# Performance work log

Hardware: AMD Instinct MI355X
Metric: run time of the kernel (lower is better)

Reference implementation:

```python
import jax, jax.numpy as jnp
import numpy as np

B = 65536      # batch (groups of time steps)
T = 5          # time_step
OBS = 128      # unit-data feature dim
ACT = 32       # action feature dim
H = 64         # n_hidden
EPS = 1e-12    # tf.contrib layer_norm epsilon
FORGET_BIAS = 1.0


def _ln_last(x, g, b):
    # layer norm over last axis (2D inputs in the TF graph)
    m = jnp.mean(x, axis=-1, keepdims=True)
    v = jnp.mean(jnp.square(x - m), axis=-1, keepdims=True)
    return (x - m) * jax.lax.rsqrt(v + EPS) * g + b


def _ln_all_but_batch(x, g, b):
    # tf.contrib.layers.layer_norm on 3D input: normalize over axes (1,2), params on last axis
    m = jnp.mean(x, axis=(1, 2), keepdims=True)
    v = jnp.mean(jnp.square(x - m), axis=(1, 2), keepdims=True)
    return (x - m) * jax.lax.rsqrt(v + EPS) * g + b


def _rev_seq(x, au):
    # tf.reverse_sequence along time axis 1 with per-batch lengths au
    t = jnp.arange(T)[None, :]
    idx = jnp.where(t < au[:, None], au[:, None] - 1 - t, t)  # [B, T]
    return jnp.take_along_axis(x, idx[:, :, None], axis=1)


def _lstm(x_btc, au, kernel, bias):
    # BasicLSTMCell (gates i, j, f, o) with sequence_length semantics:
    # past the length, outputs are zero and state is copied through.
    x_tbc = jnp.transpose(x_btc, (1, 0, 2))  # [T, B, C]
    Bn = x_tbc.shape[1]
    c0 = jnp.zeros((Bn, H), x_btc.dtype)
    h0 = jnp.zeros((Bn, H), x_btc.dtype)

    def step(carry, inp):
        c, h = carry
        x_t, t = inp
        valid = (t < au)[:, None]
        gates = jnp.concatenate([x_t, h], axis=-1) @ kernel + bias
        i, j, f, o = jnp.split(gates, 4, axis=-1)
        new_c = jax.nn.sigmoid(f + FORGET_BIAS) * c + jax.nn.sigmoid(i) * jnp.tanh(j)
        new_h = jax.nn.sigmoid(o) * jnp.tanh(new_c)
        c = jnp.where(valid, new_c, c)
        h_carry = jnp.where(valid, new_h, h)
        out = jnp.where(valid, new_h, 0.0)
        return (c, h_carry), out

    (_, _), ys = jax.lax.scan(step, (c0, h0), (x_tbc, jnp.arange(T)))
    return jnp.transpose(ys, (1, 0, 2))  # [B, T, H]


def setup_inputs() -> dict:
    key = jax.random.key(0)
    ks = jax.random.split(key, 12)
    s = 0.05
    return {
        "ud": jax.random.normal(ks[0], (B * T, OBS), jnp.float32),
        "action": jax.random.normal(ks[1], (B * T, ACT), jnp.float32),
        "mask": jax.random.uniform(ks[2], (B, T), jnp.float32),
        "ln0_g": jnp.ones((OBS,), jnp.float32), "ln0_b": jnp.zeros((OBS,), jnp.float32),
        "W1": jax.random.normal(ks[3], (OBS, H), jnp.float32) * s, "b1": jnp.zeros((H,), jnp.float32),
        "ln1_g": jnp.ones((H,), jnp.float32), "ln1_b": jnp.zeros((H,), jnp.float32),
        "W2": jax.random.normal(ks[4], (H + ACT, H), jnp.float32) * s, "b2": jnp.zeros((H,), jnp.float32),
        "ln2_g": jnp.ones((H,), jnp.float32), "ln2_b": jnp.zeros((H,), jnp.float32),
        "fw_k": jax.random.normal(ks[5], (2 * H, 4 * H), jnp.float32) * s,
        "fw_b": jnp.zeros((4 * H,), jnp.float32),
        "bw_k": jax.random.normal(ks[6], (2 * H, 4 * H), jnp.float32) * s,
        "bw_b": jnp.zeros((4 * H,), jnp.float32),
        "ln3_g": jnp.ones((2 * H,), jnp.float32), "ln3_b": jnp.zeros((2 * H,), jnp.float32),
        "conv_w": jax.random.uniform(ks[7], (2 * H,), jnp.float32, -0.003, 0.003),
        "conv_b": jnp.zeros((), jnp.float32),
        "au": jax.random.randint(ks[8], (B,), 1, T + 1, jnp.int32),
    }


def reference(ud, action, mask, ln0_g, ln0_b, W1, b1, ln1_g, ln1_b, W2, b2,
              ln2_g, ln2_b, fw_k, fw_b, bw_k, bw_b, ln3_g, ln3_b,
              conv_w, conv_b, au):
    x = _ln_last(ud, ln0_g, ln0_b)
    x = x @ W1 + b1
    x = jax.nn.relu(_ln_last(x, ln1_g, ln1_b))
    x = jnp.concatenate([x, action], axis=-1)
    x = x @ W2 + b2
    x = jax.nn.relu(_ln_last(x, ln2_g, ln2_b))
    x = x.reshape(B, T, H)
    fw = _lstm(x, au, fw_k, fw_b)
    bw = _rev_seq(_lstm(_rev_seq(x, au), au, bw_k, bw_b), au)
    x = jnp.concatenate([fw, bw], axis=2)                     # [B, T, 2H]
    x = jax.nn.relu(_ln_all_but_batch(x, ln3_g, ln3_b))
    # conv1d with kernel_size=stride=2H on [B, T*2H, 1] == per-step dot product
    q = jnp.einsum('btc,c->bt', x, conv_w) + conv_b           # [B, T]
    Q_mask = q * mask
    Q = jnp.sum(Q_mask, axis=1, keepdims=True)                # [B, 1]
    return Q


if __name__ == "__main__":
    out = reference(**setup_inputs())
    print(out.shape)
```

## Files before the change

kernel.cpp:

```cpp
#include <hip/hip_runtime.h>
#include <hip/hip_bf16.h>

#define NB    65536
#define NT    5
#define NOBS  128
#define NACT  32
#define NH    64

typedef __attribute__((ext_vector_type(8))) short bf16x8;
typedef __attribute__((ext_vector_type(4))) float f32x4;

__device__ __forceinline__ float sigf(float x) { return 1.0f / (1.0f + __expf(-x)); }
__device__ __forceinline__ float tanh_fast(float x) { return 1.0f - 2.0f / (__expf(2.0f * x) + 1.0f); }

__device__ __forceinline__ unsigned short f2b(float x) {
  __hip_bfloat16 h = __float2bfloat16(x);
  return *(unsigned short*)&h;
}
__device__ __forceinline__ float b2f(unsigned short u) {
  __hip_bfloat16 h = *(__hip_bfloat16*)&u;
  return __bfloat162float(h);
}
__device__ __forceinline__ void split_bf16(float x, unsigned short& h, unsigned short& l) {
  h = f2b(x);
  l = f2b(x - b2f(h));
}

__global__ __launch_bounds__(256) void k0_prep(
    const float* __restrict__ fk, const float* __restrict__ bk,
    const float* __restrict__ W1, const float* __restrict__ W2,
    const float* __restrict__ ln0g, const float* __restrict__ ln0b,
    const float* __restrict__ b1,
    unsigned int* __restrict__ fkT, unsigned int* __restrict__ bkT,
    unsigned short* __restrict__ w1h, unsigned short* __restrict__ w1l,
    unsigned short* __restrict__ w2h, unsigned short* __restrict__ w2l,
    float* __restrict__ u1, float* __restrict__ vb1) {
  const int bx = blockIdx.x;
  if (bx < 64) {
    const int g  = threadIdx.x;
    const int k0 = bx * 2;
    unsigned int flo = f2b(fk[(k0 + 0) * 256 + g]);
    unsigned int fhi = f2b(fk[(k0 + 1) * 256 + g]);
    unsigned int blo = f2b(bk[(k0 + 0) * 256 + g]);
    unsigned int bhi = f2b(bk[(k0 + 1) * 256 + g]);
    fkT[g * 64 + bx] = flo | (fhi << 16);
    bkT[g * 64 + bx] = blo | (bhi << 16);
    return;
  }
  const int id = (bx - 64) * 256 + threadIdx.x;
  if (id < 1024) {
    const int f = id >> 6, l = id & 63;
    const int kb = f >> 2, nt = f & 3;
    const int q = l >> 4, l16 = l & 15;
    const int n = nt * 16 + l16;
    bf16x8 vh, vl;
#pragma unroll
    for (int j = 0; j < 8; ++j) {
      const int k = kb * 32 + q * 8 + j;
      float wg = ln0g[k] * W1[k * 64 + n];
      unsigned short h, lo;
      split_bf16(wg, h, lo);
      vh[j] = (short)h; vl[j] = (short)lo;
    }
    *(bf16x8*)&w1h[(f * 64 + l) * 8] = vh;
    *(bf16x8*)&w1l[(f * 64 + l) * 8] = vl;
  } else if (id < 1792) {
    const int f = (id - 1024) >> 6, l = id & 63;
    const int kb = f >> 2, nt = f & 3;
    const int q = l >> 4, l16 = l & 15;
    const int n = nt * 16 + l16;
    bf16x8 vh, vl;
#pragma unroll
    for (int j = 0; j < 8; ++j) {
      const int k = kb * 32 + q * 8 + j;
      float wv = W2[k * 64 + n];
      unsigned short h, lo;
      split_bf16(wv, h, lo);
      vh[j] = (short)h; vl[j] = (short)lo;
    }
    *(bf16x8*)&w2h[(f * 64 + l) * 8] = vh;
    *(bf16x8*)&w2l[(f * 64 + l) * 8] = vl;
  } else if (id < 1856) {
    const int n = id - 1792;
    float u = 0.0f, vb = 0.0f;
    for (int k = 0; k < 128; ++k) {
      float wv = W1[k * 64 + n];
      u  += ln0g[k] * wv;
      vb += ln0b[k] * wv;
    }
    u1[n]  = u;
    vb1[n] = vb + b1[n];
  }
}

__global__ __launch_bounds__(256, 2) void k1_mlp(
    const float* __restrict__ ud, const float* __restrict__ action,
    const unsigned short* __restrict__ w1h, const unsigned short* __restrict__ w1l,
    const unsigned short* __restrict__ w2h, const unsigned short* __restrict__ w2l,
    const float* __restrict__ u1, const float* __restrict__ vb1,
    const float* __restrict__ gb2, const float* __restrict__ ln1g,
    const float* __restrict__ ln1b, const float* __restrict__ ln2g,
    const float* __restrict__ ln2b,
    unsigned short* __restrict__ hin) {
  const int wave = threadIdx.x >> 6;
  const int lane = threadIdx.x & 63;
  const int quad = lane >> 4;
  const int l16  = lane & 15;
  const int base = (blockIdx.x * 4 + wave) * 16;

  __shared__ __align__(16) unsigned short lds[4][4][2048];
  unsigned short* xh  = &lds[wave][0][0];
  unsigned short* xl  = &lds[wave][1][0];
  unsigned short* x2h = &lds[wave][2][0];
  unsigned short* x2l = &lds[wave][3][0];

  float u1v[4], vbv[4], g1v[4], c1v[4], b2v[4], g2v[4], c2v[4];
#pragma unroll
  for (int nt = 0; nt < 4; ++nt) {
    const int col = nt * 16 + l16;
    u1v[nt] = u1[col];  vbv[nt] = vb1[col];
    g1v[nt] = ln1g[col]; c1v[nt] = ln1b[col];
    b2v[nt] = gb2[col];
    g2v[nt] = ln2g[col]; c2v[nt] = ln2b[col];
  }

  {
    const int arow = lane >> 2, ag = lane & 3;
    const float* ap = &action[(size_t)(base + arow) * NACT + ag * 8];
    float4 a0 = *(const float4*)ap;
    float4 a1 = *(const float4*)(ap + 4);
    float av[8] = {a0.x, a0.y, a0.z, a0.w, a1.x, a1.y, a1.z, a1.w};
    bf16x8 vh, vl;
#pragma unroll
    for (int j = 0; j < 8; ++j) {
      unsigned short h, lo;
      split_bf16(av[j], h, lo);
      vh[j] = (short)h; vl[j] = (short)lo;
    }
    const int idx = arow * 128 + (((8 + ag) ^ (arow & 15)) << 3);
    *(bf16x8*)&x2h[idx] = vh;
    *(bf16x8*)&x2l[idx] = vl;
  }

#pragma unroll
  for (int r = 0; r < 16; ++r) {
    float2 xx = *(const float2*)&ud[(size_t)(base + r) * NOBS + 2 * lane];
    unsigned short h0, l0, h1, l1;
    split_bf16(xx.x, h0, l0);
    split_bf16(xx.y, h1, l1);
    const int di = r * 64 + (((lane >> 2) ^ (r & 15)) << 2) + (lane & 3);
    ((unsigned int*)xh)[di] = (unsigned int)h0 | ((unsigned int)h1 << 16);
    ((unsigned int*)xl)[di] = (unsigned int)l0 | ((unsigned int)l1 << 16);
  }

  bf16x8 W1hf[16], W1lf[16];
#pragma unroll
  for (int f = 0; f < 16; ++f) {
    W1hf[f] = *(const bf16x8*)&w1h[(f * 64 + lane) * 8];
    W1lf[f] = *(const bf16x8*)&w1l[(f * 64 + lane) * 8];
  }

  bf16x8 ones;
#pragma unroll
  for (int j = 0; j < 8; ++j) ones[j] = (short)0x3F80;

  f32x4 acc[4], s_acc, q_acc;
#pragma unroll
  for (int nt = 0; nt < 4; ++nt) acc[nt] = 0.0f;
  s_acc = 0.0f; q_acc = 0.0f;

#pragma unroll
  for (int kb = 0; kb < 4; ++kb) {
    const int ai = l16 * 128 + (((kb * 4 + quad) ^ l16) << 3);
    bf16x8 Ah = *(const bf16x8*)&xh[ai];
    bf16x8 Al = *(const bf16x8*)&xl[ai];
    bf16x8 Asq;
#pragma unroll
    for (int j = 0; j < 8; ++j) {
      unsigned int uu = ((unsigned int)(unsigned short)Ah[j]) << 16;
      float v = __uint_as_float(uu);
      v *= v;
      Asq[j] = (short)(unsigned short)(__float_as_uint(v) >> 16);
    }
    s_acc = __builtin_amdgcn_mfma_f32_16x16x32_bf16(Ah, ones, s_acc, 0, 0, 0);
    s_acc = __builtin_amdgcn_mfma_f32_16x16x32_bf16(Al, ones, s_acc, 0, 0, 0);
    q_acc = __builtin_amdgcn_mfma_f32_16x16x32_bf16(Asq, ones, q_acc, 0, 0, 0);
#pragma unroll
    for (int nt = 0; nt < 4; ++nt) {
      const int f = kb * 4 + nt;
      acc[nt] = __builtin_amdgcn_mfma_f32_16x16x32_bf16(Ah, W1hf[f], acc[nt], 0, 0, 0);
      acc[nt] = __builtin_amdgcn_mfma_f32_16x16x32_bf16(Ah, W1lf[f], acc[nt], 0, 0, 0);
      acc[nt] = __builtin_amdgcn_mfma_f32_16x16x32_bf16(Al, W1hf[f], acc[nt], 0, 0, 0);
    }
  }

  float inv0[4], ivm[4];
#pragma unroll
  for (int r = 0; r < 4; ++r) {
    float m   = s_acc[r] * (1.0f / 128.0f);
    float var = q_acc[r] * (1.0f / 128.0f) - m * m;
    float inv = rsqrtf(var + 1e-12f);
    inv0[r] = inv;
    ivm[r]  = inv * m;
  }
  float y[4][4];
#pragma unroll
  for (int nt = 0; nt < 4; ++nt)
#pragma unroll
    for (int r = 0; r < 4; ++r)
      y[nt][r] = fmaf(inv0[r], acc[nt][r], fmaf(-ivm[r], u1v[nt], vbv[nt]));

  float m1[4], i1[4];
#pragma unroll
  for (int r = 0; r < 4; ++r) {
    float s1 = y[0][r] + y[1][r] + y[2][r] + y[3][r];
    float q1 = y[0][r] * y[0][r] + y[1][r] * y[1][r] +
               y[2][r] * y[2][r] + y[3][r] * y[3][r];
#pragma unroll
    for (int off = 1; off <= 8; off <<= 1) {
      s1 += __shfl_xor(s1, off, 64);
      q1 += __shfl_xor(q1, off, 64);
    }
    float mm = s1 * (1.0f / 64.0f);
    m1[r] = mm;
    i1[r] = rsqrtf(q1 * (1.0f / 64.0f) - mm * mm + 1e-12f);
  }

#pragma unroll
  for (int nt = 0; nt < 4; ++nt)
#pragma unroll
    for (int r = 0; r < 4; ++r) {
      float x1 = fmaxf(0.0f, fmaf((y[nt][r] - m1[r]) * i1[r], g1v[nt], c1v[nt]));
      unsigned short h, lo;
      split_bf16(x1, h, lo);
      const int row = quad * 4 + r;
      const int idx = row * 128 + (((nt * 2 + (l16 >> 3)) ^ (row & 15)) << 3) + (l16 & 7);
      x2h[idx] = h;
      x2l[idx] = lo;
    }

  f32x4 acc2[4];
#pragma unroll
  for (int nt = 0; nt < 4; ++nt) acc2[nt] = 0.0f;

#pragma unroll
  for (int kb = 0; kb < 3; ++kb) {
    bf16x8 w2hf[4], w2lf[4];
#pragma unroll
    for (int nt = 0; nt < 4; ++nt) {
      const int f = kb * 4 + nt;
      w2hf[nt] = *(const bf16x8*)&w2h[(f * 64 + lane) * 8];
      w2lf[nt] = *(const bf16x8*)&w2l[(f * 64 + lane) * 8];
    }
    const int ai = l16 * 128 + (((kb * 4 + quad) ^ l16) << 3);
    bf16x8 Ah = *(const bf16x8*)&x2h[ai];
    bf16x8 Al = *(const bf16x8*)&x2l[ai];
#pragma unroll
    for (int nt = 0; nt < 4; ++nt) {
      acc2[nt] = __builtin_amdgcn_mfma_f32_16x16x32_bf16(Ah, w2hf[nt], acc2[nt], 0, 0, 0);
      acc2[nt] = __builtin_amdgcn_mfma_f32_16x16x32_bf16(Ah, w2lf[nt], acc2[nt], 0, 0, 0);
      acc2[nt] = __builtin_amdgcn_mfma_f32_16x16x32_bf16(Al, w2hf[nt], acc2[nt], 0, 0, 0);
    }
  }

  float y2[4][4];
#pragma unroll
  for (int nt = 0; nt < 4; ++nt)
#pragma unroll
    for (int r = 0; r < 4; ++r)
      y2[nt][r] = acc2[nt][r] + b2v[nt];

  float m2[4], i2[4];
#pragma unroll
  for (int r = 0; r < 4; ++r) {
    float s2 = y2[0][r] + y2[1][r] + y2[2][r] + y2[3][r];
    float q2 = y2[0][r] * y2[0][r] + y2[1][r] * y2[1][r] +
               y2[2][r] * y2[2][r] + y2[3][r] * y2[3][r];
#pragma unroll
    for (int off = 1; off <= 8; off <<= 1) {
      s2 += __shfl_xor(s2, off, 64);
      q2 += __shfl_xor(q2, off, 64);
    }
    float mm = s2 * (1.0f / 64.0f);
    m2[r] = mm;
    i2[r] = rsqrtf(q2 * (1.0f / 64.0f) - mm * mm + 1e-12f);
  }

#pragma unroll
  for (int nt = 0; nt < 4; ++nt)
#pragma unroll
    for (int r = 0; r < 4; ++r) {
      float o = fmaxf(0.0f, fmaf((y2[nt][r] - m2[r]) * i2[r], g2v[nt], c2v[nt]));
      const int row = quad * 4 + r;
      hin[(size_t)(base + row) * NH + nt * 16 + l16] = f2b(o);
    }
}

__global__ __launch_bounds__(256, 2) void k23_lstm_final(
    const unsigned short* __restrict__ hin,
    const unsigned short* __restrict__ fkT, const float* __restrict__ fwb,
    const unsigned short* __restrict__ bkT, const float* __restrict__ bwb,
    const int* __restrict__ au,
    const float* __restrict__ ln3g, const float* __restrict__ ln3b,
    const float* __restrict__ conv_w, const float* __restrict__ conv_b,
    const float* __restrict__ mask, float* __restrict__ out) {
  const int tid  = threadIdx.x;
  const int w    = tid >> 6;
  const int lane = tid & 63;
  const int quad = lane >> 4;
  const int l16  = lane & 15;
  const int batch0 = blockIdx.x * 32;

  __shared__ __align__(16) unsigned short obuf[10 * 32 * 64];
  __shared__ __align__(16) unsigned short hA[32 * 64];

  const int u = w * 16 + l16;

  const int aum0 = au[batch0 + l16];
  const int aum1 = au[batch0 + 16 + l16];
  int aur[8];
#pragma unroll
  for (int mt = 0; mt < 2; ++mt)
#pragma unroll
    for (int r = 0; r < 4; ++r)
      aur[mt * 4 + r] = au[batch0 + mt * 16 + quad * 4 + r];

  for (int dir = 0; dir < 2; ++dir) {
    const unsigned short* kT   = dir ? bkT : fkT;
    const float*          bias = dir ? bwb : fwb;

    bf16x8 Bf[4][4];
#pragma unroll
    for (int g = 0; g < 4; ++g) {
      const int n = g * 64 + u;
#pragma unroll
      for (int kb = 0; kb < 4; ++kb)
        Bf[g][kb] = *(const bf16x8*)&kT[n * 128 + kb * 32 + quad * 8];
    }
    const float bg0 = bias[u], bg1 = bias[64 + u];
    const float bg2 = bias[128 + u], bg3 = bias[192 + u];

    __syncthreads();
    *(float4*)&hA[tid * 8] = make_float4(0.f, 0.f, 0.f, 0.f);
    float c_s[8], h_s[8];
#pragma unroll
    for (int i = 0; i < 8; ++i) { c_s[i] = 0.0f; h_s[i] = 0.0f; }
    __syncthreads();

    bf16x8 Ax0[2], Ax1[2];
#pragma unroll
    for (int mt = 0; mt < 2; ++mt) {
      const int m = mt * 16 + l16;
      const int a = mt ? aum1 : aum0;
      const int st = dir ? (a - 1) : 0;
      const size_t rb = ((size_t)(batch0 + m) * NT + st) * NH;
      Ax0[mt] = *(const bf16x8*)&hin[rb + quad * 8];
      Ax1[mt] = *(const bf16x8*)&hin[rb + 32 + quad * 8];
    }

    for (int t = 0; t < NT; ++t) {
      f32x4 acc[2][4];
#pragma unroll
      for (int mt = 0; mt < 2; ++mt)
#pragma unroll
        for (int g = 0; g < 4; ++g) acc[mt][g] = 0.0f;

#pragma unroll
      for (int mt = 0; mt < 2; ++mt) {
        const int m = mt * 16 + l16;
        bf16x8 Ah0 = *(const bf16x8*)&hA[m * 64 + ((quad ^ (m & 7)) << 3)];
        bf16x8 Ah1 = *(const bf16x8*)&hA[m * 64 + (((4 + quad) ^ (m & 7)) << 3)];
#pragma unroll
        for (int g = 0; g < 4; ++g) {
          acc[mt][g] = __builtin_amdgcn_mfma_f32_16x16x32_bf16(Ax0[mt], Bf[g][0], acc[mt][g], 0, 0, 0);
          acc[mt][g] = __builtin_amdgcn_mfma_f32_16x16x32_bf16(Ax1[mt], Bf[g][1], acc[mt][g], 0, 0, 0);
          acc[mt][g] = __builtin_amdgcn_mfma_f32_16x16x32_bf16(Ah0, Bf[g][2], acc[mt][g], 0, 0, 0);
          acc[mt][g] = __builtin_amdgcn_mfma_f32_16x16x32_bf16(Ah1, Bf[g][3], acc[mt][g], 0, 0, 0);
        }
      }

      if (t < NT - 1) {
        const int t2 = t + 1;
#pragma unroll
        for (int mt = 0; mt < 2; ++mt) {
          const int m = mt * 16 + l16;
          const int a = mt ? aum1 : aum0;
          const int st = dir ? ((t2 < a) ? (a - 1 - t2) : t2) : t2;
          const size_t rb = ((size_t)(batch0 + m) * NT + st) * NH;
          Ax0[mt] = *(const bf16x8*)&hin[rb + quad * 8];
          Ax1[mt] = *(const bf16x8*)&hin[rb + 32 + quad * 8];
        }
      }

      __syncthreads();

#pragma unroll
      for (int mt = 0; mt < 2; ++mt) {
#pragma unroll
        for (int r = 0; r < 4; ++r) {
          const int idx = mt * 4 + r;
          const int bl = mt * 16 + quad * 4 + r;
          float gi = acc[mt][0][r] + bg0;
          float gj = acc[mt][1][r] + bg1;
          float gf = acc[mt][2][r] + bg2;
          float go = acc[mt][3][r] + bg3;
          float nc = sigf(gf + 1.0f) * c_s[idx] + sigf(gi) * tanh_fast(gj);
          float nh = sigf(go) * tanh_fast(nc);
          bool valid = t < aur[idx];
          c_s[idx] = valid ? nc : c_s[idx];
          h_s[idx] = valid ? nh : h_s[idx];
          float outv = valid ? nh : 0.0f;
          int pos = dir ? ((t < aur[idx]) ? (aur[idx] - 1 - t) : t) : t;
          obuf[(dir * 5 + pos) * 2048 + bl * 64 + u] = f2b(outv);
          hA[bl * 64 + (((u >> 3) ^ (bl & 7)) << 3) + (u & 7)] = f2b(h_s[idx]);
        }
      }
      __syncthreads();
    }
  }

  const float gl  = ln3g[lane],      gh  = ln3g[64 + lane];
  const float bl3 = ln3b[lane],      bh3 = ln3b[64 + lane];
  const float cwl = conv_w[lane],    cwh = conv_w[64 + lane];
  const float cb  = conv_b[0];

  for (int bb = w * 8; bb < w * 8 + 8; ++bb) {
    const int b = batch0 + bb;
    float v0[NT], v1[NT];
#pragma unroll
    for (int p = 0; p < NT; ++p) {
      v0[p] = b2f(obuf[p * 2048 + bb * 64 + lane]);
      v1[p] = b2f(obuf[(5 + p) * 2048 + bb * 64 + lane]);
    }
    float s = 0.0f, q = 0.0f;
#pragma unroll
    for (int p = 0; p < NT; ++p) {
      s += v0[p] + v1[p];
      q += v0[p] * v0[p] + v1[p] * v1[p];
    }
#pragma unroll
    for (int off = 32; off; off >>= 1) {
      s += __shfl_xor(s, off, 64);
      q += __shfl_xor(q, off, 64);
    }
    float m = s * (1.0f / 640.0f);
    float var = q * (1.0f / 640.0f) - m * m;
    float inv = rsqrtf(var + 1e-12f);

    float mk[NT], masksum = 0.0f;
#pragma unroll
    for (int p = 0; p < NT; ++p) {
      mk[p] = mask[b * NT + p];
      masksum += mk[p];
    }
    float local = 0.0f;
#pragma unroll
    for (int p = 0; p < NT; ++p) {
      float xf = fmaxf(0.0f, (v0[p] - m) * inv * gl + bl3);
      float xb = fmaxf(0.0f, (v1[p] - m) * inv * gh + bh3);
      local += mk[p] * (xf * cwl + xb * cwh);
    }
#pragma unroll
    for (int off = 32; off; off >>= 1) local += __shfl_xor(local, off, 64);
    if (lane == 0) out[b] = local + cb * masksum;
  }
}

extern "C" void kernel_launch(void* const* d_in, const int* in_sizes, int n_in,
                              void* d_out, int out_size, void* d_ws, size_t ws_size,
                              hipStream_t stream) {
  const float* ud     = (const float*)d_in[0];
  const float* action = (const float*)d_in[1];
  const float* mask   = (const float*)d_in[2];
  const float* ln0g   = (const float*)d_in[3];
  const float* ln0b   = (const float*)d_in[4];
  const float* W1     = (const float*)d_in[5];
  const float* b1     = (const float*)d_in[6];
  const float* ln1g   = (const float*)d_in[7];
  const float* ln1b   = (const float*)d_in[8];
  const float* W2     = (const float*)d_in[9];
  const float* b2     = (const float*)d_in[10];
  const float* ln2g   = (const float*)d_in[11];
  const float* ln2b   = (const float*)d_in[12];
  const float* fwk    = (const float*)d_in[13];
  const float* fwb    = (const float*)d_in[14];
  const float* bwk    = (const float*)d_in[15];
  const float* bwb    = (const float*)d_in[16];
  const float* ln3g   = (const float*)d_in[17];
  const float* ln3b   = (const float*)d_in[18];
  const float* conv_w = (const float*)d_in[19];
  const float* conv_b = (const float*)d_in[20];
  const int*   au     = (const int*)d_in[21];

  const size_t n_hin = (size_t)NB * NT * NH;
  unsigned short* wsu   = (unsigned short*)d_ws;
  unsigned short* hin   = wsu;
  unsigned short* fkT   = hin + n_hin;
  unsigned short* bkT   = fkT + 32768;
  unsigned short* w1h   = bkT + 32768;
  unsigned short* w1l   = w1h + 8192;
  unsigned short* w2h   = w1l + 8192;
  unsigned short* w2l   = w2h + 6144;
  float*          u1    = (float*)(w2l + 6144);
  float*          vb1   = u1 + 64;

  float* outf = (float*)d_out;

  k0_prep<<<72, 256, 0, stream>>>(fwk, bwk, W1, W2, ln0g, ln0b, b1,
                                  (unsigned int*)fkT, (unsigned int*)bkT,
                                  w1h, w1l, w2h, w2l, u1, vb1);
  k1_mlp<<<(NB * NT) / 64, 256, 0, stream>>>(ud, action, w1h, w1l, w2h, w2l,
                                             u1, vb1, b2, ln1g, ln1b, ln2g, ln2b,
                                             hin);
  k23_lstm_final<<<NB / 32, 256, 0, stream>>>(hin, fkT, fwb, bkT, bwb, au,
                                              ln3g, ln3b, conv_w, conv_b,
                                              mask, outf);
}
```

Before: 515.9 us.

## Double-buffer LSTM hidden state, fold biases into MFMA init, use fast rcp and raise occupancy

Double-buffers the shared hidden-state tile so each timestep needs one barrier instead of two, and drops the barrier before zeroing the state. The gate biases, including the forget bias, now seed the MFMA accumulators, and sigmoid/tanh use the hardware reciprocal. The output and hidden values are packed to bf16 with a single instruction. Launch bounds go from 2 to 3 blocks per SM, which may force register spills given the large weight fragments held in registers. The final layer-norm/conv epilogue is unrolled to handle two batch rows per iteration so their shuffle reductions interleave.

Result: slower. 562.2 us (+9.0%).

```diff
diff --git a/kernel.cpp b/kernel.cpp
--- a/kernel.cpp
+++ b/kernel.cpp
@@ -10,8 +10,9 @@
 typedef __attribute__((ext_vector_type(8))) short bf16x8;
 typedef __attribute__((ext_vector_type(4))) float f32x4;
 
-__device__ __forceinline__ float sigf(float x) { return 1.0f / (1.0f + __expf(-x)); }
-__device__ __forceinline__ float tanh_fast(float x) { return 1.0f - 2.0f / (__expf(2.0f * x) + 1.0f); }
+__device__ __forceinline__ float rcp_fast(float x) { return __builtin_amdgcn_rcpf(x); }
+__device__ __forceinline__ float sigf(float x) { return rcp_fast(1.0f + __expf(-x)); }
+__device__ __forceinline__ float tanh_fast(float x) { return 1.0f - 2.0f * rcp_fast(__expf(2.0f * x) + 1.0f); }
 
 __device__ __forceinline__ unsigned short f2b(float x) {
   __hip_bfloat16 h = __float2bfloat16(x);
@@ -296,7 +297,7 @@
     }
 }
 
-__global__ __launch_bounds__(256, 2) void k23_lstm_final(
+__global__ __launch_bounds__(256, 3) void k23_lstm_final(
     const unsigned short* __restrict__ hin,
     const unsigned short* __restrict__ fkT, const float* __restrict__ fwb,
     const unsigned short* __restrict__ bkT, const float* __restrict__ bwb,
@@ -312,7 +313,7 @@
   const int batch0 = blockIdx.x * 32;
 
   __shared__ __align__(16) unsigned short obuf[10 * 32 * 64];
-  __shared__ __align__(16) unsigned short hA[32 * 64];
+  __shared__ __align__(16) unsigned short hA[2][32 * 64];
 
   const int u = w * 16 + l16;
 
@@ -338,10 +339,9 @@
         Bf[g][kb] = *(const bf16x8*)&kT[n * 128 + kb * 32 + quad * 8];
     }
     const float bg0 = bias[u], bg1 = bias[64 + u];
-    const float bg2 = bias[128 + u], bg3 = bias[192 + u];
-
-    __syncthreads();
-    *(float4*)&hA[tid * 8] = make_float4(0.f, 0.f, 0.f, 0.f);
+    const float bg2 = bias[128 + u] + 1.0f, bg3 = bias[192 + u];
+
+    *(float4*)&hA[0][tid * 8] = make_float4(0.f, 0.f, 0.f, 0.f);
     float c_s[8], h_s[8];
 #pragma unroll
     for (int i = 0; i < 8; ++i) { c_s[i] = 0.0f; h_s[i] = 0.0f; }
@@ -358,18 +358,20 @@
       Ax1[mt] = *(const bf16x8*)&hin[rb + 32 + quad * 8];
     }
 
+    int cur = 0;
     for (int t = 0; t < NT; ++t) {
+      const int nxt = cur ^ 1;
       f32x4 acc[2][4];
 #pragma unroll
-      for (int mt = 0; mt < 2; ++mt)
-#pragma unroll
-        for (int g = 0; g < 4; ++g) acc[mt][g] = 0.0f;
+      for (int mt = 0; mt < 2; ++mt) {
+        acc[mt][0] = bg0; acc[mt][1] = bg1; acc[mt][2] = bg2; acc[mt][3] = bg3;
+      }
 
 #pragma unroll
       for (int mt = 0; mt < 2; ++mt) {
         const int m = mt * 16 + l16;
-        bf16x8 Ah0 = *(const bf16x8*)&hA[m * 64 + ((quad ^ (m & 7)) << 3)];
-        bf16x8 Ah1 = *(const bf16x8*)&hA[m * 64 + (((4 + quad) ^ (m & 7)) << 3)];
+        bf16x8 Ah0 = *(const bf16x8*)&hA[cur][m * 64 + ((quad ^ (m & 7)) << 3)];
+        bf16x8 Ah1 = *(const bf16x8*)&hA[cur][m * 64 + (((4 + quad) ^ (m & 7)) << 3)];
 #pragma unroll
         for (int g = 0; g < 4; ++g) {
           acc[mt][g] = __builtin_amdgcn_mfma_f32_16x16x32_bf16(Ax0[mt], Bf[g][0], acc[mt][g], 0, 0, 0);
@@ -392,30 +394,33 @@
         }
       }
 
-      __syncthreads();
-
 #pragma unroll
       for (int mt = 0; mt < 2; ++mt) {
 #pragma unroll
         for (int r = 0; r < 4; ++r) {
           const int idx = mt * 4 + r;
           const int bl = mt * 16 + quad * 4 + r;
-          float gi = acc[mt][0][r] + bg0;
-          float gj = acc[mt][1][r] + bg1;
-          float gf = acc[mt][2][r] + bg2;
-          float go = acc[mt][3][r] + bg3;
-          float nc = sigf(gf + 1.0f) * c_s[idx] + sigf(gi) * tanh_fast(gj);
+          const int a  = aur[idx];
+          float gi = acc[mt][0][r];
+          float gj = acc[mt][1][r];
+          float gf = acc[mt][2][r];
+          float go = acc[mt][3][r];
+          float nc = sigf(gf) * c_s[idx] + sigf(gi) * tanh_fast(gj);
           float nh = sigf(go) * tanh_fast(nc);
-          bool valid = t < aur[idx];
+          bool valid = t < a;
           c_s[idx] = valid ? nc : c_s[idx];
           h_s[idx] = valid ? nh : h_s[idx];
           float outv = valid ? nh : 0.0f;
-          int pos = dir ? ((t < aur[idx]) ? (aur[idx] - 1 - t) : t) : t;
-          obuf[(dir * 5 + pos) * 2048 + bl * 64 + u] = f2b(outv);
-          hA[bl * 64 + (((u >> 3) ^ (bl & 7)) << 3) + (u & 7)] = f2b(h_s[idx]);
+          int pos = dir ? (valid ? (a - 1 - t) : t) : t;
+          unsigned int pk;
+          asm("v_cvt_pk_bf16_f32 %0, %1, %2" : "=v"(pk) : "v"(outv), "v"(h_s[idx]));
+          obuf[(dir * 5 + pos) * 2048 + bl * 64 + u] = (unsigned short)pk;
+          hA[nxt][bl * 64 + (((u >> 3) ^ (bl & 7)) << 3) + (u & 7)] =
+              (unsigned short)(pk >> 16);
         }
       }
       __syncthreads();
+      cur = nxt;
     }
   }
 
@@ -424,45 +429,59 @@
   const float cwl = conv_w[lane],    cwh = conv_w[64 + lane];
   const float cb  = conv_b[0];
 
-  for (int bb = w * 8; bb < w * 8 + 8; ++bb) {
-    const int b = batch0 + bb;
-    float v0[NT], v1[NT];
-#pragma unroll
-    for (int p = 0; p < NT; ++p) {
-      v0[p] = b2f(obuf[p * 2048 + bb * 64 + lane]);
-      v1[p] = b2f(obuf[(5 + p) * 2048 + bb * 64 + lane]);
-    }
-    float s = 0.0f, q = 0.0f;
-#pragma unroll
-    for (int p = 0; p < NT; ++p) {
-      s += v0[p] + v1[p];
-      q += v0[p] * v0[p] + v1[p] * v1[p];
+  for (int bb = w * 8; bb < w * 8 + 8; bb += 2) {
+    float v0[2][NT], v1[2][NT];
+#pragma unroll
+    for (int u2 = 0; u2 < 2; ++u2)
+#pragma unroll
+      for (int p = 0; p < NT; ++p) {
+        v0[u2][p] = b2f(obuf[p * 2048 + (bb + u2) * 64 + lane]);
+        v1[u2][p] = b2f(obuf[(5 + p) * 2048 + (bb + u2) * 64 + lane]);
+      }
+    float s[2], q[2];
+#pragma unroll
+    for (int u2 = 0; u2 < 2; ++u2) {
+      s[u2] = 0.0f; q[u2] = 0.0f;
+#pragma unroll
+      for (int p = 0; p < NT; ++p) {
+        s[u2] += v0[u2][p] + v1[u2][p];
+        q[u2] += v0[u2][p] * v0[u2][p] + v1[u2][p] * v1[u2][p];
+      }
     }
 #pragma unroll
     for (int off = 32; off; off >>= 1) {
-      s += __shfl_xor(s, off, 64);
-      q += __shfl_xor(q, off, 64);
-    }
-    float m = s * (1.0f / 640.0f);
-    float var = q * (1.0f / 640.0f) - m * m;
-    float inv = rsqrtf(var + 1e-12f);
-
-    float mk[NT], masksum = 0.0f;
-#pragma unroll
-    for (int p = 0; p < NT; ++p) {
-      mk[p] = mask[b * NT + p];
-      masksum += mk[p];
-    }
-    float local = 0.0f;
-#pragma unroll
-    for (int p = 0; p < NT; ++p) {
-      float xf = fmaxf(0.0f, (v0[p] - m) * inv * gl + bl3);
-      float xb = fmaxf(0.0f, (v1[p] - m) * inv * gh + bh3);
-      local += mk[p] * (xf * cwl + xb * cwh);
-    }
-#pragma unroll
-    for (int off = 32; off; off >>= 1) local += __shfl_xor(local, off, 64);
-    if (lane == 0) out[b] = local + cb * masksum;
+      s[0] += __shfl_xor(s[0], off, 64);
+      q[0] += __shfl_xor(q[0], off, 64);
+      s[1] += __shfl_xor(s[1], off, 64);
+      q[1] += __shfl_xor(q[1], off, 64);
+    }
+    float local[2], msum[2];
+#pragma unroll
+    for (int u2 = 0; u2 < 2; ++u2) {
+      const int b = batch0 + bb + u2;
+      float m   = s[u2] * (1.0f / 640.0f);
+      float var = q[u2] * (1.0f / 640.0f) - m * m;
+      float inv = __builtin_amdgcn_rsqf(var + 1e-12f);
+      float acc = 0.0f, ms = 0.0f;
+#pragma unroll
+      for (int p = 0; p < NT; ++p) {
+        float mk = mask[b * NT + p];
+        ms += mk;
+        float xf = fmaxf(0.0f, (v0[u2][p] - m) * inv * gl + bl3);
+        float xb = fmaxf(0.0f, (v1[u2][p] - m) * inv * gh + bh3);
+        acc += mk * (xf * cwl + xb * cwh);
+      }
+      local[u2] = acc; msum[u2] = ms;
+    }
+#pragma unroll
+    for (int off = 32; off; off >>= 1) {
+      local[0] += __shfl_xor(local[0], off, 64);
+      local[1] += __shfl_xor(local[1], off, 64);
+    }
+    if (lane == 0) {
+      out[batch0 + bb]     = local[0] + cb * msum[0];
+      out[batch0 + bb + 1] = local[1] + cb * msum[1];
+    }
   }
 }
 
```
